# Kernel optimization log

Hardware: AMD Instinct MI355X
Metric: run time of the kernel (lower is better)

The kernel has to match this reference:

```python
import jax, jax.numpy as jnp
import numpy as np

N_NODES = 20000
N_EDGES = 160000
F_IN = 128
H1 = 1024  # 128 * out_channels
H2 = 512   # 64 * out_channels
OUT = 8    # out_channels


def graph_conv(x, src, dst, w_rel, b_rel, w_root):
    # PyG GraphConv(aggr='mean'): out = lin_rel(mean_{j->i} x_j) + lin_root(x_i)
    n = x.shape[0]
    agg = jax.ops.segment_sum(x[src], dst, num_segments=n)          # [N, F_in]
    deg = jax.ops.segment_sum(jnp.ones((src.shape[0],), x.dtype), dst, num_segments=n)
    mean = agg / jnp.maximum(deg, 1.0)[:, None]
    return mean @ w_rel + b_rel + x @ w_root


def setup_inputs() -> dict:
    key = jax.random.key(0)
    ks = jax.random.split(key, 12)
    x = jax.random.normal(ks[0], (N_NODES, F_IN), dtype=jnp.float32)
    edge_index = jax.random.randint(ks[1], (2, N_EDGES), 0, N_NODES, dtype=jnp.int64)

    def lin(k, fi, fo):
        return jax.random.normal(k, (fi, fo), dtype=jnp.float32) / np.sqrt(fi)

    return {
        "x": x,
        "edge_index": edge_index,
        "w1_rel": lin(ks[2], F_IN, H1), "b1": jnp.zeros((H1,), jnp.float32), "w1_root": lin(ks[3], F_IN, H1),
        "w2_rel": lin(ks[4], H1, H2), "b2": jnp.zeros((H2,), jnp.float32), "w2_root": lin(ks[5], H1, H2),
        "wmu_rel": lin(ks[6], H2, OUT), "bmu": jnp.zeros((OUT,), jnp.float32), "wmu_root": lin(ks[7], H2, OUT),
        "wls_rel": lin(ks[8], H2, OUT), "bls": jnp.zeros((OUT,), jnp.float32), "wls_root": lin(ks[9], H2, OUT),
    }


def reference(x, edge_index, w1_rel, b1, w1_root, w2_rel, b2, w2_root,
              wmu_rel, bmu, wmu_root, wls_rel, bls, wls_root):
    src, dst = edge_index[0], edge_index[1]
    h = jax.nn.relu(graph_conv(x, src, dst, w1_rel, b1, w1_root))
    h = jax.nn.relu(graph_conv(h, src, dst, w2_rel, b2, w2_root))
    mu = graph_conv(h, src, dst, wmu_rel, bmu, wmu_root)
    logstd = graph_conv(h, src, dst, wls_rel, bls, wls_root)
    return (mu, logstd)
```

## Files before the change

### kernel.cpp

```cpp
#include <hip/hip_runtime.h>

typedef __attribute__((ext_vector_type(8))) short short8;
typedef __attribute__((ext_vector_type(4))) float f32x4;
typedef unsigned long long u64;

__device__ __forceinline__ unsigned short f2bf(float f) {
  union { float f; unsigned u; } v; v.f = f;
  unsigned u = v.u;
  unsigned r = (u + 0x7FFFu + ((u >> 16) & 1u)) >> 16;
  return (unsigned short)r;
}
__device__ __forceinline__ float bf2f(unsigned short s) {
  union { unsigned u; float f; } v; v.u = ((unsigned)s) << 16;
  return v.f;
}

__device__ __forceinline__ void gl_lds16(const unsigned short* g, unsigned short* l) {
  __builtin_amdgcn_global_load_lds(
      (const __attribute__((address_space(1))) void*)g,
      (__attribute__((address_space(3))) void*)l, 16, 0, 0);
}


__global__ void init_kernel(int* a, int n, int* b, int nb, int* flag,
                            const long long* edges, int nslots, int n_nodes) {
  int i = blockIdx.x * blockDim.x + threadIdx.x;
  int stride = gridDim.x * blockDim.x;
  for (int j = i; j < n; j += stride) a[j] = 0;
  for (int j = i; j < nb; j += stride) b[j] = 0;
  if (i == 0) *flag = 1;
  for (int j = i; j < nslots; j += stride) {
    long long v = edges[j];
    if (v < 0 || v >= n_nodes) atomicAnd(flag, 0);
  }
}

__device__ __forceinline__ int edge_at(const void* p, int is64, size_t idx) {
  return is64 ? (int)((const long long*)p)[idx] : ((const int*)p)[idx];
}

__global__ void count_kernel(const void* edges, int E, const int* flag, int* deg) {
  int is64 = *flag;
  int i = blockIdx.x * blockDim.x + threadIdx.x;
  int stride = gridDim.x * blockDim.x;
  for (int e = i; e < E; e += stride) {
    int d = edge_at(edges, is64, (size_t)E + e);
    atomicAdd(&deg[d], 1);
  }
}

__global__ void scan_kernel(const int* __restrict__ deg, int* __restrict__ rs,
                            float* __restrict__ invdeg, int n) {
  __shared__ int ssum[1024];
  int tid = threadIdx.x;
  int chunk = (n + 1023) >> 10;
  int start = tid * chunk;
  int end = min(start + chunk, n);
  int s = 0;
  for (int i = start; i < end; ++i) s += deg[i];
  ssum[tid] = s;
  __syncthreads();
  for (int off = 1; off < 1024; off <<= 1) {
    int t = (tid >= off) ? ssum[tid - off] : 0;
    __syncthreads();
    ssum[tid] += t;
    __syncthreads();
  }
  int run = (tid ? ssum[tid - 1] : 0);
  if (tid == 0) rs[0] = 0;
  for (int i = start; i < end; ++i) {
    int d = deg[i];
    run += d;
    rs[i + 1] = run;
    invdeg[i] = 1.0f / fmaxf((float)d, 1.0f);
  }
}

__global__ void fill_kernel(const void* edges, int E, const int* flag,
                            const int* __restrict__ rs, int* cursor, int* col_src) {
  int is64 = *flag;
  int i = blockIdx.x * blockDim.x + threadIdx.x;
  int stride = gridDim.x * blockDim.x;
  for (int e = i; e < E; e += stride) {
    int d = edge_at(edges, is64, (size_t)E + e);
    int s = edge_at(edges, is64, (size_t)e);
    int p = atomicAdd(&cursor[d], 1);
    col_src[rs[d] + p] = s;
  }
}


__global__ void agg1_kernel(const float* __restrict__ x,
                            const int* __restrict__ rs, const int* __restrict__ cs,
                            const float* __restrict__ invdeg,
                            unsigned short* __restrict__ A1) {
  int node = blockIdx.x;
  int f = threadIdx.x;
  float xi = x[(size_t)node * 128 + f];
  float acc = 0.f;
  int e1 = rs[node + 1];
  for (int e = rs[node]; e < e1; ++e) {
    acc += x[(size_t)cs[e] * 128 + f];
  }
  A1[(size_t)node * 256 + f] = f2bf(acc * invdeg[node]);
  A1[(size_t)node * 256 + 128 + f] = f2bf(xi);
}

__global__ void agg2_kernel(const unsigned short* __restrict__ P2,
                            const int* __restrict__ rs, const int* __restrict__ cs,
                            const float* __restrict__ invdeg,
                            const float* __restrict__ b2,
                            unsigned short* __restrict__ h2, int M) {
  int node = blockIdx.x * 2 + (threadIdx.x >> 6);
  if (node >= M) return;
  int f0 = (threadIdx.x & 63) * 8;
  float acc[8];
#pragma unroll
  for (int v = 0; v < 8; ++v) acc[v] = 0.f;
  int e1 = rs[node + 1];
  for (int e = rs[node]; e < e1; ++e) {
    int s = cs[e];
    uint4 w = *reinterpret_cast<const uint4*>(P2 + (size_t)s * 1024 + f0);
    acc[0] += bf2f((unsigned short)(w.x & 0xffff));
    acc[1] += bf2f((unsigned short)(w.x >> 16));
    acc[2] += bf2f((unsigned short)(w.y & 0xffff));
    acc[3] += bf2f((unsigned short)(w.y >> 16));
    acc[4] += bf2f((unsigned short)(w.z & 0xffff));
    acc[5] += bf2f((unsigned short)(w.z >> 16));
    acc[6] += bf2f((unsigned short)(w.w & 0xffff));
    acc[7] += bf2f((unsigned short)(w.w >> 16));
  }
  float inv = invdeg[node];
  uint4 wr = *reinterpret_cast<const uint4*>(P2 + (size_t)node * 1024 + 512 + f0);
  float rt[8] = {
    bf2f((unsigned short)(wr.x & 0xffff)), bf2f((unsigned short)(wr.x >> 16)),
    bf2f((unsigned short)(wr.y & 0xffff)), bf2f((unsigned short)(wr.y >> 16)),
    bf2f((unsigned short)(wr.z & 0xffff)), bf2f((unsigned short)(wr.z >> 16)),
    bf2f((unsigned short)(wr.w & 0xffff)), bf2f((unsigned short)(wr.w >> 16))};
  unsigned short o[8];
#pragma unroll
  for (int v = 0; v < 8; ++v)
    o[v] = f2bf(fmaxf(acc[v] * inv + rt[v] + b2[f0 + v], 0.f));
  uint4 pk;
  pk.x = (unsigned)o[0] | ((unsigned)o[1] << 16);
  pk.y = (unsigned)o[2] | ((unsigned)o[3] << 16);
  pk.z = (unsigned)o[4] | ((unsigned)o[5] << 16);
  pk.w = (unsigned)o[6] | ((unsigned)o[7] << 16);
  *reinterpret_cast<uint4*>(h2 + (size_t)node * 512 + f0) = pk;
}

__global__ void head_agg_kernel(const float* __restrict__ P3,
                                const int* __restrict__ rs, const int* __restrict__ cs,
                                const float* __restrict__ invdeg,
                                const float* __restrict__ bmu, const float* __restrict__ bls,
                                float* __restrict__ outmu, float* __restrict__ outls, int M) {
  int idx = blockIdx.x * blockDim.x + threadIdx.x;
  int node = idx >> 4;
  int c = idx & 15;
  if (node >= M) return;
  int relc = (c < 8) ? c : (16 + (c - 8));
  float acc = 0.f;
  int e1 = rs[node + 1];
  for (int e = rs[node]; e < e1; ++e) acc += P3[(size_t)cs[e] * 128 + relc];
  float v = acc * invdeg[node] + P3[(size_t)node * 128 + relc + 8]
          + ((c < 8) ? bmu[c] : bls[c - 8]);
  if (c < 8) outmu[(size_t)node * 8 + c] = v;
  else outls[(size_t)node * 8 + (c - 8)] = v;
}


__device__ __forceinline__ void ttile(const float* __restrict__ src, int Nw,
                                      unsigned short* __restrict__ dst, int ldd,
                                      int rowoff, int coloff,
                                      int tileIdx, int tilesN, float (*tile)[33]) {
  int tk = tileIdx / tilesN, tn = tileIdx % tilesN;
  int k0 = tk * 32, n0 = tn * 32;
  int tx = threadIdx.x & 31, ty = threadIdx.x >> 5;
#pragma unroll
  for (int s = 0; s < 4; ++s)
    tile[ty + s * 8][tx] = src[(size_t)(k0 + ty + s * 8) * Nw + n0 + tx];
  __syncthreads();
#pragma unroll
  for (int s = 0; s < 4; ++s)
    dst[(size_t)(rowoff + n0 + ty + s * 8) * ldd + coloff + k0 + tx] =
        f2bf(tile[tx][ty + s * 8]);
}

__global__ void wtrans_all_kernel(const float* __restrict__ w1_rel, const float* __restrict__ w1_root,
                                  const float* __restrict__ w2_rel, const float* __restrict__ w2_root,
                                  const float* __restrict__ wmu_rel, const float* __restrict__ wmu_root,
                                  const float* __restrict__ wls_rel, const float* __restrict__ wls_root,
                                  unsigned short* __restrict__ Bt1,
                                  unsigned short* __restrict__ Bt2,
                                  unsigned short* __restrict__ Bt3) {
  __shared__ float tile[32][33];
  int b = blockIdx.x;
  if (b < 128)       ttile(w1_rel, 1024, Bt1, 256, 0, 0, b, 32, tile);
  else if (b < 256)  ttile(w1_root, 1024, Bt1, 256, 0, 128, b - 128, 32, tile);
  else if (b < 768)  ttile(w2_rel, 512, Bt2, 1024, 0, 0, b - 256, 16, tile);
  else if (b < 1280) ttile(w2_root, 512, Bt2, 1024, 512, 0, b - 768, 16, tile);
  else {
    int idx = (b - 1280) * 256 + threadIdx.x;
    int n = idx >> 9, k = idx & 511;
    float v;
    if (n < 8) v = wmu_rel[(size_t)k * 8 + n];
    else if (n < 16) v = wmu_root[(size_t)k * 8 + (n - 8)];
    else if (n < 24) v = wls_rel[(size_t)k * 8 + (n - 16)];
    else v = wls_root[(size_t)k * 8 + (n - 24)];
    Bt3[(size_t)n * 512 + k] = f2bf(v);
  }
}

__launch_bounds__(256, 4)
__global__ void gemm_db_kernel(const unsigned short* __restrict__ A, int lda,
                               const unsigned short* __restrict__ Bt, int ldb,
                               const float* __restrict__ bias,
                               void* __restrict__ outp, int ldo,
                               int M, int N, int K, int relu, int out_f32, int gx) {
  __shared__ unsigned short As[2 * 4096];
  __shared__ unsigned short Bs[2 * 4096];
  const int tid = threadIdx.x;
  const int lane = tid & 63;
  const int w = tid >> 6;
  const int wr = w >> 1, wc = w & 1;
  const int lr = lane & 15, lk = lane >> 4;
  const int sw8 = (lk ^ ((lr >> 1) & 3)) * 8;

  int nwg = gridDim.x, orig = blockIdx.x;
  int q = nwg >> 3, r = nwg & 7;
  int xcd = orig & 7, lid = orig >> 3;
  int swz = (xcd < r ? xcd * (q + 1) : r * (q + 1) + (xcd - r) * q) + lid;
  int m0 = (swz / gx) * 128, n0 = (swz % gx) * 128;

  f32x4 acc[4][4];
#pragma unroll
  for (int i = 0; i < 4; ++i)
#pragma unroll
    for (int j = 0; j < 4; ++j) acc[i][j] = (f32x4)0.0f;

  const int r0 = tid >> 2;
  const int slog = ((tid & 3) ^ ((r0 >> 1) & 3)) * 8;
  const unsigned short* gA = A + (size_t)(m0 + r0) * lda + slog;
  const unsigned short* gB = Bt + (size_t)(n0 + r0) * ldb + slog;
  const size_t a64 = (size_t)64 * lda, b64 = (size_t)64 * ldb;
  unsigned short* wa = As + w * 512;
  unsigned short* wb = Bs + w * 512;

  auto STG = [&](int s, int t) {
    const unsigned short* a = gA + (size_t)t * 32;
    const unsigned short* b = gB + (size_t)t * 32;
    gl_lds16(a, wa + s * 4096);
    gl_lds16(a + a64, wa + s * 4096 + 2048);
    gl_lds16(b, wb + s * 4096);
    gl_lds16(b + b64, wb + s * 4096 + 2048);
  };

  const int nt = K >> 5;
  STG(0, 0);
  asm volatile("s_waitcnt vmcnt(0)" ::: "memory");
  __builtin_amdgcn_s_barrier();

  int buf = 0;
  for (int t = 0; t < nt; ++t) {
    if (t + 1 < nt) STG(buf ^ 1, t + 1);
    const unsigned short* as_ = As + buf * 4096;
    const unsigned short* bs_ = Bs + buf * 4096;
    short8 af[4], bf[4];
#pragma unroll
    for (int i = 0; i < 4; ++i) {
      af[i] = *reinterpret_cast<const short8*>(&as_[(wr * 64 + i * 16 + lr) * 32 + sw8]);
      bf[i] = *reinterpret_cast<const short8*>(&bs_[(wc * 64 + i * 16 + lr) * 32 + sw8]);
    }
    __builtin_amdgcn_s_setprio(1);
#pragma unroll
    for (int i = 0; i < 4; ++i)
#pragma unroll
      for (int j = 0; j < 4; ++j)
        acc[i][j] = __builtin_amdgcn_mfma_f32_16x16x32_bf16(af[i], bf[j], acc[i][j], 0, 0, 0);
    __builtin_amdgcn_s_setprio(0);
    if (t + 1 < nt) {
      asm volatile("s_waitcnt vmcnt(0) lgkmcnt(0)" ::: "memory");
      __builtin_amdgcn_s_barrier();
    }
    buf ^= 1;
  }

#pragma unroll
  for (int i = 0; i < 4; ++i) {
    int row_b = m0 + wr * 64 + i * 16 + lk * 4;
#pragma unroll
    for (int j = 0; j < 4; ++j) {
      int col = n0 + wc * 64 + j * 16 + lr;
      float bv = bias ? bias[col] : 0.f;
#pragma unroll
      for (int rr = 0; rr < 4; ++rr) {
        int row = row_b + rr;
        if (row < M) {
          float v = acc[i][j][rr] + bv;
          if (relu) v = fmaxf(v, 0.f);
          if (out_f32) ((float*)outp)[(size_t)row * ldo + col] = v;
          else ((unsigned short*)outp)[(size_t)row * ldo + col] = f2bf(v);
        }
      }
    }
  }
}


extern "C" void kernel_launch(void* const* d_in, const int* in_sizes, int n_in,
                              void* d_out, int out_size, void* d_ws, size_t ws_size,
                              hipStream_t stream) {
  const float* x = (const float*)d_in[0];
  const void* edge = d_in[1];
  const float* w1_rel = (const float*)d_in[2];
  const float* b1 = (const float*)d_in[3];
  const float* w1_root = (const float*)d_in[4];
  const float* w2_rel = (const float*)d_in[5];
  const float* b2 = (const float*)d_in[6];
  const float* w2_root = (const float*)d_in[7];
  const float* wmu_rel = (const float*)d_in[8];
  const float* bmu = (const float*)d_in[9];
  const float* wmu_root = (const float*)d_in[10];
  const float* wls_rel = (const float*)d_in[11];
  const float* bls = (const float*)d_in[12];
  const float* wls_root = (const float*)d_in[13];

  const int FIN = 128, H1 = 1024, H2 = 512;
  const int M = in_sizes[0] / FIN;
  const int E = in_sizes[1] / 2;
  const int Mpad = ((M + 127) / 128) * 128;
  const int gy = Mpad / 128;

  char* ws = (char*)d_ws;
  size_t off = 0;
  auto alloc = [&](size_t bytes) -> char* {
    char* p = ws + off;
    off = (off + bytes + 255) & ~(size_t)255;
    return p;
  };
  int* flag = (int*)alloc(4);
  int* deg = (int*)alloc((size_t)M * 4);
  int* cursor = (int*)alloc((size_t)M * 4);
  int* rs = (int*)alloc((size_t)(M + 1) * 4);
  float* invdeg = (float*)alloc((size_t)M * 4);
  int* cs = (int*)alloc((size_t)E * 4);
  unsigned short* A1 = (unsigned short*)alloc((size_t)Mpad * 256 * 2);
  unsigned short* h1 = (unsigned short*)alloc((size_t)Mpad * 1024 * 2);
  unsigned short* P2 = (unsigned short*)alloc((size_t)Mpad * 1024 * 2);
  unsigned short* h2 = (unsigned short*)alloc((size_t)Mpad * 512 * 2);
  float* P3 = (float*)alloc((size_t)Mpad * 128 * 4);
  unsigned short* Bt1 = (unsigned short*)alloc((size_t)H1 * 256 * 2);
  unsigned short* Bt2 = (unsigned short*)alloc((size_t)1024 * 1024 * 2);
  unsigned short* Bt3 = (unsigned short*)alloc((size_t)128 * 512 * 2);

  init_kernel<<<64, 256, 0, stream>>>(deg, M, cursor, M, flag, (const long long*)edge, 2048, M);
  count_kernel<<<256, 256, 0, stream>>>(edge, E, flag, deg);
  scan_kernel<<<1, 1024, 0, stream>>>(deg, rs, invdeg, M);
  fill_kernel<<<256, 256, 0, stream>>>(edge, E, flag, rs, cursor, cs);

  wtrans_all_kernel<<<1344, 256, 0, stream>>>(w1_rel, w1_root, w2_rel, w2_root,
                                              wmu_rel, wmu_root, wls_rel, wls_root,
                                              Bt1, Bt2, Bt3);

  agg1_kernel<<<M, 128, 0, stream>>>(x, rs, cs, invdeg, A1);
  gemm_db_kernel<<<(H1 / 128) * gy, 256, 0, stream>>>(
      A1, 256, Bt1, 256, b1, h1, 1024, M, H1, 256, 1, 0, H1 / 128);

  gemm_db_kernel<<<(1024 / 128) * gy, 256, 0, stream>>>(
      h1, 1024, Bt2, 1024, nullptr, P2, 1024, M, 1024, 1024, 0, 0, 1024 / 128);
  agg2_kernel<<<(M + 1) / 2, 128, 0, stream>>>(P2, rs, cs, invdeg, b2, h2, M);

  gemm_db_kernel<<<1 * gy, 256, 0, stream>>>(
      h2, 512, Bt3, 512, nullptr, P3, 128, M, 128, 512, 0, 1, 1);
  float* outmu = (float*)d_out;
  float* outls = outmu + (size_t)M * 8;
  head_agg_kernel<<<(M * 16 + 255) / 256, 256, 0, stream>>>(
      P3, rs, cs, invdeg, bmu, bls, outmu, outls, M);
}
```

Before: 281.3 us.

## Add narrow 32-column head GEMM and merge init with weight transpose

```diff
diff --git a/kernel.cpp b/kernel.cpp
--- a/kernel.cpp
+++ b/kernel.cpp
@@ -22,15 +22,60 @@
 }
 
 
-__global__ void init_kernel(int* a, int n, int* b, int nb, int* flag,
-                            const long long* edges, int nslots, int n_nodes) {
+__device__ __forceinline__ void ttile(const float* __restrict__ src, int Nw,
+                                      unsigned short* __restrict__ dst, int ldd,
+                                      int rowoff, int coloff,
+                                      int tileIdx, int tilesN, float (*tile)[33]) {
+  int tk = tileIdx / tilesN, tn = tileIdx % tilesN;
+  int k0 = tk * 32, n0 = tn * 32;
+  int tx = threadIdx.x & 31, ty = threadIdx.x >> 5;
+#pragma unroll
+  for (int s = 0; s < 4; ++s)
+    tile[ty + s * 8][tx] = src[(size_t)(k0 + ty + s * 8) * Nw + n0 + tx];
+  __syncthreads();
+#pragma unroll
+  for (int s = 0; s < 4; ++s)
+    dst[(size_t)(rowoff + n0 + ty + s * 8) * ldd + coloff + k0 + tx] =
+        f2bf(tile[tx][ty + s * 8]);
+}
+
+__global__ void prep_kernel(int* deg, int* cursor, int n, int* flag,
+                            const float* __restrict__ w1_rel, const float* __restrict__ w1_root,
+                            const float* __restrict__ w2_rel, const float* __restrict__ w2_root,
+                            const float* __restrict__ wmu_rel, const float* __restrict__ wmu_root,
+                            const float* __restrict__ wls_rel, const float* __restrict__ wls_root,
+                            unsigned short* __restrict__ Bt1,
+                            unsigned short* __restrict__ Bt2,
+                            unsigned short* __restrict__ Bt3) {
+  __shared__ float tile[32][33];
+  int b = blockIdx.x;
+  if (b >= 1344) {
+    int i = (b - 1344) * blockDim.x + threadIdx.x;
+    int stride = 64 * blockDim.x;
+    for (int j = i; j < n; j += stride) { deg[j] = 0; cursor[j] = 0; }
+    if (i == 0) *flag = 1;
+    return;
+  }
+  if (b < 128)       ttile(w1_rel, 1024, Bt1, 256, 0, 0, b, 32, tile);
+  else if (b < 256)  ttile(w1_root, 1024, Bt1, 256, 0, 128, b - 128, 32, tile);
+  else if (b < 768)  ttile(w2_rel, 512, Bt2, 1024, 0, 0, b - 256, 16, tile);
+  else if (b < 1280) ttile(w2_root, 512, Bt2, 1024, 512, 0, b - 768, 16, tile);
+  else {
+    int idx = (b - 1280) * 256 + threadIdx.x;
+    int nn = idx >> 9, k = idx & 511;
+    float v;
+    if (nn < 8) v = wmu_rel[(size_t)k * 8 + nn];
+    else if (nn < 16) v = wmu_root[(size_t)k * 8 + (nn - 8)];
+    else if (nn < 24) v = wls_rel[(size_t)k * 8 + (nn - 16)];
+    else v = wls_root[(size_t)k * 8 + (nn - 24)];
+    Bt3[(size_t)nn * 512 + k] = f2bf(v);
+  }
+}
+
+__global__ void detect_kernel(const long long* p, int nslots, int n_nodes, int* flag) {
   int i = blockIdx.x * blockDim.x + threadIdx.x;
-  int stride = gridDim.x * blockDim.x;
-  for (int j = i; j < n; j += stride) a[j] = 0;
-  for (int j = i; j < nb; j += stride) b[j] = 0;
-  if (i == 0) *flag = 1;
-  for (int j = i; j < nslots; j += stride) {
-    long long v = edges[j];
+  if (i < nslots) {
+    long long v = p[i];
     if (v < 0 || v >= n_nodes) atomicAnd(flag, 0);
   }
 }
@@ -161,54 +206,11 @@
   int relc = (c < 8) ? c : (16 + (c - 8));
   float acc = 0.f;
   int e1 = rs[node + 1];
-  for (int e = rs[node]; e < e1; ++e) acc += P3[(size_t)cs[e] * 128 + relc];
-  float v = acc * invdeg[node] + P3[(size_t)node * 128 + relc + 8]
+  for (int e = rs[node]; e < e1; ++e) acc += P3[(size_t)cs[e] * 32 + relc];
+  float v = acc * invdeg[node] + P3[(size_t)node * 32 + relc + 8]
           + ((c < 8) ? bmu[c] : bls[c - 8]);
   if (c < 8) outmu[(size_t)node * 8 + c] = v;
   else outls[(size_t)node * 8 + (c - 8)] = v;
-}
-
-
-__device__ __forceinline__ void ttile(const float* __restrict__ src, int Nw,
-                                      unsigned short* __restrict__ dst, int ldd,
-                                      int rowoff, int coloff,
-                                      int tileIdx, int tilesN, float (*tile)[33]) {
-  int tk = tileIdx / tilesN, tn = tileIdx % tilesN;
-  int k0 = tk * 32, n0 = tn * 32;
-  int tx = threadIdx.x & 31, ty = threadIdx.x >> 5;
-#pragma unroll
-  for (int s = 0; s < 4; ++s)
-    tile[ty + s * 8][tx] = src[(size_t)(k0 + ty + s * 8) * Nw + n0 + tx];
-  __syncthreads();
-#pragma unroll
-  for (int s = 0; s < 4; ++s)
-    dst[(size_t)(rowoff + n0 + ty + s * 8) * ldd + coloff + k0 + tx] =
-        f2bf(tile[tx][ty + s * 8]);
-}
-
-__global__ void wtrans_all_kernel(const float* __restrict__ w1_rel, const float* __restrict__ w1_root,
-                                  const float* __restrict__ w2_rel, const float* __restrict__ w2_root,
-                                  const float* __restrict__ wmu_rel, const float* __restrict__ wmu_root,
-                                  const float* __restrict__ wls_rel, const float* __restrict__ wls_root,
-                                  unsigned short* __restrict__ Bt1,
-                                  unsigned short* __restrict__ Bt2,
-                                  unsigned short* __restrict__ Bt3) {
-  __shared__ float tile[32][33];
-  int b = blockIdx.x;
-  if (b < 128)       ttile(w1_rel, 1024, Bt1, 256, 0, 0, b, 32, tile);
-  else if (b < 256)  ttile(w1_root, 1024, Bt1, 256, 0, 128, b - 128, 32, tile);
-  else if (b < 768)  ttile(w2_rel, 512, Bt2, 1024, 0, 0, b - 256, 16, tile);
-  else if (b < 1280) ttile(w2_root, 512, Bt2, 1024, 512, 0, b - 768, 16, tile);
-  else {
-    int idx = (b - 1280) * 256 + threadIdx.x;
-    int n = idx >> 9, k = idx & 511;
-    float v;
-    if (n < 8) v = wmu_rel[(size_t)k * 8 + n];
-    else if (n < 16) v = wmu_root[(size_t)k * 8 + (n - 8)];
-    else if (n < 24) v = wls_rel[(size_t)k * 8 + (n - 16)];
-    else v = wls_root[(size_t)k * 8 + (n - 24)];
-    Bt3[(size_t)n * 512 + k] = f2bf(v);
-  }
 }
 
 __launch_bounds__(256, 4)
@@ -301,6 +303,91 @@
           if (out_f32) ((float*)outp)[(size_t)row * ldo + col] = v;
           else ((unsigned short*)outp)[(size_t)row * ldo + col] = f2bf(v);
         }
+      }
+    }
+  }
+}
+
+__launch_bounds__(256, 3)
+__global__ void gemm_heads_kernel(const unsigned short* __restrict__ A,
+                                  const unsigned short* __restrict__ Bt3,
+                                  float* __restrict__ P3, int M, int gx_unused) {
+  __shared__ unsigned short Bs[16 * 1024];
+  __shared__ unsigned short As[2 * 4096];
+  const int tid = threadIdx.x;
+  const int lane = tid & 63;
+  const int w = tid >> 6;
+  const int lr = lane & 15, lk = lane >> 4;
+  const int sw8 = (lk ^ ((lr >> 1) & 3)) * 8;
+
+  int nwg = gridDim.x, orig = blockIdx.x;
+  int q = nwg >> 3, r = nwg & 7;
+  int xcd = orig & 7, lid = orig >> 3;
+  int swz = (xcd < r ? xcd * (q + 1) : r * (q + 1) + (xcd - r) * q) + lid;
+  int m0 = swz * 128;
+
+  for (int i = 0; i < 8; ++i) {
+    int j = i * 256 + tid;
+    int n = j >> 6, p = j & 63;
+    int x = (n >> 1) & 3;
+    uint4 v = *reinterpret_cast<const uint4*>(Bt3 + (size_t)n * 512 + ((p & ~3) | ((p & 3) ^ x)) * 8);
+    *reinterpret_cast<uint4*>(&Bs[(p >> 2) * 1024 + n * 32 + (p & 3) * 8]) = v;
+  }
+
+  f32x4 acc[2][2];
+#pragma unroll
+  for (int i = 0; i < 2; ++i)
+#pragma unroll
+    for (int j = 0; j < 2; ++j) acc[i][j] = (f32x4)0.0f;
+
+  const int r0 = tid >> 2;
+  const int slog = ((tid & 3) ^ ((r0 >> 1) & 3)) * 8;
+  const unsigned short* gA = A + (size_t)(m0 + r0) * 512 + slog;
+  const size_t a64 = (size_t)64 * 512;
+  unsigned short* wa = As + w * 512;
+
+  auto STG = [&](int s, int t) {
+    const unsigned short* a = gA + (size_t)t * 32;
+    gl_lds16(a, wa + s * 4096);
+    gl_lds16(a + a64, wa + s * 4096 + 2048);
+  };
+
+  STG(0, 0);
+  __syncthreads();
+
+  int buf = 0;
+  const int nt = 16;
+  for (int t = 0; t < nt; ++t) {
+    if (t + 1 < nt) STG(buf ^ 1, t + 1);
+    const unsigned short* as_ = As + buf * 4096;
+    short8 af[2], bf[2];
+#pragma unroll
+    for (int i = 0; i < 2; ++i) {
+      af[i] = *reinterpret_cast<const short8*>(&as_[(w * 32 + i * 16 + lr) * 32 + sw8]);
+      bf[i] = *reinterpret_cast<const short8*>(&Bs[t * 1024 + (i * 16 + lr) * 32 + sw8]);
+    }
+#pragma unroll
+    for (int i = 0; i < 2; ++i)
+#pragma unroll
+      for (int j = 0; j < 2; ++j)
+        acc[i][j] = __builtin_amdgcn_mfma_f32_16x16x32_bf16(af[i], bf[j], acc[i][j], 0, 0, 0);
+    if (t + 1 < nt) {
+      asm volatile("s_waitcnt vmcnt(0) lgkmcnt(0)" ::: "memory");
+      __builtin_amdgcn_s_barrier();
+    }
+    buf ^= 1;
+  }
+
+#pragma unroll
+  for (int i = 0; i < 2; ++i) {
+    int row_b = m0 + w * 32 + i * 16 + lk * 4;
+#pragma unroll
+    for (int j = 0; j < 2; ++j) {
+      int col = j * 16 + lr;
+#pragma unroll
+      for (int rr = 0; rr < 4; ++rr) {
+        int row = row_b + rr;
+        if (row < M) P3[(size_t)row * 32 + col] = acc[i][j][rr];
       }
     }
   }
@@ -348,20 +435,20 @@
   unsigned short* h1 = (unsigned short*)alloc((size_t)Mpad * 1024 * 2);
   unsigned short* P2 = (unsigned short*)alloc((size_t)Mpad * 1024 * 2);
   unsigned short* h2 = (unsigned short*)alloc((size_t)Mpad * 512 * 2);
-  float* P3 = (float*)alloc((size_t)Mpad * 128 * 4);
+  float* P3 = (float*)alloc((size_t)Mpad * 32 * 4);
   unsigned short* Bt1 = (unsigned short*)alloc((size_t)H1 * 256 * 2);
   unsigned short* Bt2 = (unsigned short*)alloc((size_t)1024 * 1024 * 2);
-  unsigned short* Bt3 = (unsigned short*)alloc((size_t)128 * 512 * 2);
-
-  init_kernel<<<64, 256, 0, stream>>>(deg, M, cursor, M, flag, (const long long*)edge, 2048, M);
+  unsigned short* Bt3 = (unsigned short*)alloc((size_t)32 * 512 * 2);
+
+  prep_kernel<<<1408, 256, 0, stream>>>(deg, cursor, M, flag,
+                                        w1_rel, w1_root, w2_rel, w2_root,
+                                        wmu_rel, wmu_root, wls_rel, wls_root,
+                                        Bt1, Bt2, Bt3);
+  detect_kernel<<<8, 256, 0, stream>>>((const long long*)edge, 2048, M, flag);
   count_kernel<<<256, 256, 0, stream>>>(edge, E, flag, deg);
   scan_kernel<<<1, 1024, 0, stream>>>(deg, rs, invdeg, M);
   fill_kernel<<<256, 256, 0, stream>>>(edge, E, flag, rs, cursor, cs);
 
-  wtrans_all_kernel<<<1344, 256, 0, stream>>>(w1_rel, w1_root, w2_rel, w2_root,
-                                              wmu_rel, wmu_root, wls_rel, wls_root,
-                                              Bt1, Bt2, Bt3);
-
   agg1_kernel<<<M, 128, 0, stream>>>(x, rs, cs, invdeg, A1);
   gemm_db_kernel<<<(H1 / 128) * gy, 256, 0, stream>>>(
       A1, 256, Bt1, 256, b1, h1, 1024, M, H1, 256, 1, 0, H1 / 128);
@@ -370,8 +457,7 @@
       h1, 1024, Bt2, 1024, nullptr, P2, 1024, M, 1024, 1024, 0, 0, 1024 / 128);
   agg2_kernel<<<(M + 1) / 2, 128, 0, stream>>>(P2, rs, cs, invdeg, b2, h2, M);
 
-  gemm_db_kernel<<<1 * gy, 256, 0, stream>>>(
-      h2, 512, Bt3, 512, nullptr, P3, 128, M, 128, 512, 0, 1, 1);
+  gemm_heads_kernel<<<gy, 256, 0, stream>>>(h2, Bt3, P3, M, 1);
   float* outmu = (float*)d_out;
   float* outls = outmu + (size_t)M * 8;
   head_agg_kernel<<<(M * 16 + 255) / 256, 256, 0, stream>>>(
```

Measured after the change: 269.6 us. 1.04x faster.
